# Performance work log

Measured on AMD Instinct MI355X. Metric: run time of the kernel, lower is better.

Reference implementation:

```python
import jax, jax.numpy as jnp
import numpy as np

WIN = 11
SIGMA = 1.5
DATA_RANGE = 2.0
C1 = (0.01 * DATA_RANGE) ** 2
C2 = (0.03 * DATA_RANGE) ** 2


def _gauss_1d():
    x = np.arange(WIN, dtype=np.float32) - WIN // 2
    g = np.exp(-(x ** 2) / (2.0 * SIGMA ** 2))
    return jnp.asarray(g / g.sum(), dtype=jnp.float32)


def _blur(x, g1d):
    c = x.shape[1]
    kh = jnp.broadcast_to(g1d.reshape(1, 1, WIN, 1), (c, 1, WIN, 1))
    kw = jnp.broadcast_to(g1d.reshape(1, 1, 1, WIN), (c, 1, 1, WIN))
    dn = ('NCHW', 'OIHW', 'NCHW')
    p = WIN // 2
    x = jax.lax.conv_general_dilated(x, kh, (1, 1), [(p, p), (0, 0)],
                                     dimension_numbers=dn, feature_group_count=c)
    x = jax.lax.conv_general_dilated(x, kw, (1, 1), [(0, 0), (p, p)],
                                     dimension_numbers=dn, feature_group_count=c)
    return x


def setup_inputs() -> dict:
    key = jax.random.key(0)
    k1, k2 = jax.random.split(key)
    shape = (32, 1, 1024, 1024)
    img1 = jax.random.normal(k1, shape, dtype=jnp.float32)
    img2 = jax.random.normal(k2, shape, dtype=jnp.float32)
    return {"img1": img1, "img2": img2}


def reference(img1, img2):
    g1d = _gauss_1d()
    mu1 = _blur(img1, g1d)
    mu2 = _blur(img2, g1d)
    mu1_sq = mu1 * mu1
    mu2_sq = mu2 * mu2
    mu1_mu2 = mu1 * mu2
    sigma1_sq = _blur(img1 * img1, g1d) - mu1_sq
    sigma2_sq = _blur(img2 * img2, g1d) - mu2_sq
    sigma12 = _blur(img1 * img2, g1d) - mu1_mu2
    ssim_map = ((2.0 * mu1_mu2 + C1) * (2.0 * sigma12 + C2)) / (
        (mu1_sq + mu2_sq + C1) * (sigma1_sq + sigma2_sq + C2))
    return 1.0 - jnp.mean(ssim_map)
```

## Files before the change

### kernel.cpp

```cpp
#include <hip/hip_runtime.h>

typedef float v2f __attribute__((ext_vector_type(2)));

namespace {
constexpr int W = 1024;
constexpr int H = 1024;
constexpr int NIMG = 32;
constexpr int SROWS = 16;
constexpr int NSTRIP = H / SROWS;
constexpr int BLOCK = 256;
constexpr int PLANE4 = 260;

constexpr float C1 = 0.0004f;
constexpr float C2 = 0.0036f;

constexpr float GW[11] = {
    0.00102838f, 0.00759876f, 0.03600077f, 0.10936070f, 0.21300554f,
    0.26601172f,
    0.21300554f, 0.10936070f, 0.03600077f, 0.00759876f, 0.00102838f};
}

__device__ __forceinline__ void lds_barrier() {
  asm volatile("s_waitcnt lgkmcnt(0)" ::: "memory");
  __builtin_amdgcn_s_barrier();
  asm volatile("" ::: "memory");
}

__device__ __forceinline__ void load_uv(const float4* __restrict__ p1,
                                        const float4* __restrict__ p2, int y,
                                        int tid, v2f uv[4]) {
  if ((unsigned)y < (unsigned)H) {
    const float4 a = p1[y * (W / 4) + tid];
    const float4 b = p2[y * (W / 4) + tid];
    uv[0] = (v2f){a.x + b.x, a.x - b.x};
    uv[1] = (v2f){a.y + b.y, a.y - b.y};
    uv[2] = (v2f){a.z + b.z, a.z - b.z};
    uv[3] = (v2f){a.w + b.w, a.w - b.w};
  } else {
#pragma unroll
    for (int c = 0; c < 4; ++c) uv[c] = (v2f){0.f, 0.f};
  }
}

__device__ __forceinline__ void hblur(const float4* __restrict__ P0,
                                      const float4* __restrict__ P1, int tid,
                                      v2f h[4]) {
  v2f t[16];
#pragma unroll
  for (int e = 0; e < 8; ++e) {
    const float4 r = (e & 1) ? P0[tid + (e + 1) / 2] : P1[tid + e / 2];
    t[2 * e + 0] = (v2f){r.x, r.y};
    t[2 * e + 1] = (v2f){r.z, r.w};
  }
#pragma unroll
  for (int m = 0; m < 4; ++m) {
    v2f s = (v2f){GW[0], GW[0]} * t[m + 1];
#pragma unroll
    for (int k = 1; k < 11; ++k)
      s = __builtin_elementwise_fma((v2f){GW[k], GW[k]}, t[m + 1 + k], s);
    h[m] = s;
  }
}

__global__ __launch_bounds__(BLOCK, 4) void ssim_main(
    const float* __restrict__ img1, const float* __restrict__ img2,
    double* __restrict__ ws) {
  __shared__ __align__(16) v2f bufUV[2][2 * PLANE4];
  __shared__ __align__(16) v2f bufSQ[2][2 * PLANE4];
  __shared__ float red[BLOCK / 64];

  const int tid = threadIdx.x;
  const int bid = blockIdx.x;
  const int img = bid / NSTRIP;
  const int strip = bid % NSTRIP;
  const int ys = strip * SROWS;

  const float4* p1 =
      reinterpret_cast<const float4*>(img1) + (size_t)img * (W / 4) * H;
  const float4* p2 =
      reinterpret_cast<const float4*>(img2) + (size_t)img * (W / 4) * H;

  if (tid < 16) {
    const int b = tid & 1, pl = (tid >> 1) & 1, si = tid >> 2;
    const int slot = (si & 1) + ((si >> 1) ? 258 : 0);
    float4* p = reinterpret_cast<float4*>(b ? bufSQ[pl] : bufUV[pl]);
    p[slot] = make_float4(0.f, 0.f, 0.f, 0.f);
  }

  v2f ruv[11][4];
#pragma unroll
  for (int s = 0; s < 10; ++s) load_uv(p1, p2, ys - 5 + s, tid, ruv[s]);
  v2f pf[4];
  load_uv(p1, p2, ys + 5, tid, pf);

  float acc = 0.f;

  for (int ii = 0; ii < SROWS; ++ii) {
#pragma unroll
    for (int c = 0; c < 4; ++c) ruv[10][c] = pf[c];
    load_uv(p1, p2, ys + ii + 6, tid, pf);

    v2f buv[4], bsq[4];
    const v2f g5 = (v2f){GW[5], GW[5]};
#pragma unroll
    for (int c = 0; c < 4; ++c) {
      const v2f x5 = ruv[5][c];
      v2f b = g5 * x5;
      v2f s = g5 * (x5 * x5);
#pragma unroll
      for (int k = 0; k < 5; ++k) {
        const v2f gk = (v2f){GW[k], GW[k]};
        const v2f xa = ruv[k][c];
        const v2f xb = ruv[10 - k][c];
        const v2f p = xa + xb;
        b = __builtin_elementwise_fma(gk, p, b);
        const v2f q = __builtin_elementwise_fma(xb, xb, xa * xa);
        s = __builtin_elementwise_fma(gk, q, s);
      }
      buv[c] = b;
      bsq[c] = s;
    }

    lds_barrier();

    {
      float4* P0 = reinterpret_cast<float4*>(bufUV[0]);
      float4* P1 = reinterpret_cast<float4*>(bufUV[1]);
      P0[tid + 2] = make_float4(buv[0].x, buv[0].y, buv[1].x, buv[1].y);
      P1[tid + 2] = make_float4(buv[2].x, buv[2].y, buv[3].x, buv[3].y);
      float4* Q0 = reinterpret_cast<float4*>(bufSQ[0]);
      float4* Q1 = reinterpret_cast<float4*>(bufSQ[1]);
      Q0[tid + 2] = make_float4(bsq[0].x, bsq[0].y, bsq[1].x, bsq[1].y);
      Q1[tid + 2] = make_float4(bsq[2].x, bsq[2].y, bsq[3].x, bsq[3].y);
    }
    lds_barrier();

    v2f huv[4], hsq[4];
    hblur(reinterpret_cast<const float4*>(bufUV[0]),
          reinterpret_cast<const float4*>(bufUV[1]), tid, huv);
    hblur(reinterpret_cast<const float4*>(bufSQ[0]),
          reinterpret_cast<const float4*>(bufSQ[1]), tid, hsq);

#pragma unroll
    for (int m = 0; m < 4; ++m) {
      const float BU = huv[m].x, BV = huv[m].y;
      const float BU2 = hsq[m].x, BV2 = hsq[m].y;
      const float P = BU * BU, Q = BV * BV;
      const float PmQ = P - Q, PpQ = P + Q;
      const float An = fmaf(0.5f, PmQ, C1);
      const float Bn = fmaf(0.5f, (BU2 - BV2) - PmQ, C2);
      const float Cd = fmaf(0.5f, PpQ, C1);
      const float Dd = fmaf(0.5f, (BU2 + BV2) - PpQ, C2);
      const float num = An * Bn;
      const float den = Cd * Dd;
      float r = __builtin_amdgcn_rcpf(den);
      r = r * fmaf(-den, r, 2.f);
      acc = fmaf(num, r, acc);
    }

#pragma unroll
    for (int k = 0; k < 10; ++k)
#pragma unroll
      for (int c = 0; c < 4; ++c) ruv[k][c] = ruv[k + 1][c];
  }

#pragma unroll
  for (int off = 32; off > 0; off >>= 1) acc += __shfl_down(acc, off, 64);
  if ((tid & 63) == 0) red[tid >> 6] = acc;
  __syncthreads();
  if (tid == 0) {
    float t = 0.f;
#pragma unroll
    for (int wv = 0; wv < BLOCK / 64; ++wv) t += red[wv];
    atomicAdd(ws, (double)t);
  }
}

__global__ void ssim_fin(const double* __restrict__ ws,
                         float* __restrict__ out) {
  out[0] =
      1.0f - (float)(ws[0] * (1.0 / ((double)NIMG * (double)W * (double)H)));
}

extern "C" void kernel_launch(void* const* d_in, const int* in_sizes, int n_in,
                              void* d_out, int out_size, void* d_ws,
                              size_t ws_size, hipStream_t stream) {
  const float* img1 = (const float*)d_in[0];
  const float* img2 = (const float*)d_in[1];
  float* out = (float*)d_out;
  double* ws = (double*)d_ws;

  hipMemsetAsync(d_ws, 0, sizeof(double), stream);
  ssim_main<<<NIMG * NSTRIP, BLOCK, 0, stream>>>(img1, img2, ws);
  ssim_fin<<<1, 1, 0, stream>>>(ws, out);
}
```

Before: 330.7 us.

## Use 512-thread blocks with 2 pixels per thread and taller strips

Each thread now handles 2 columns instead of 4 and loads float2 instead of float4, so a block has 512 threads, and each block covers 32 rows instead of 16. The LDS layout changes to one interleaved float4 plane per quantity, so the horizontal blur reads 7 float4 per thread rather than 8. Taller strips lower the vertical halo reload overhead (10 extra rows per 32 rather than per 16), and fewer registers per thread allow more waves in flight. In exchange the grid has half as many blocks, each thread does less work per row, and the horizontal pass re-reads more overlapping LDS data relative to the output it produces.

New measurement: 352.5 us. +6.6%, slower.

```diff
diff --git a/kernel.cpp b/kernel.cpp
--- a/kernel.cpp
+++ b/kernel.cpp
@@ -6,10 +6,10 @@
 constexpr int W = 1024;
 constexpr int H = 1024;
 constexpr int NIMG = 32;
-constexpr int SROWS = 16;
+constexpr int SROWS = 32;
 constexpr int NSTRIP = H / SROWS;
-constexpr int BLOCK = 256;
-constexpr int PLANE4 = 260;
+constexpr int BLOCK = 512;
+constexpr int NF4 = 520;
 
 constexpr float C1 = 0.0004f;
 constexpr float C2 = 0.0036f;
@@ -26,34 +26,31 @@
   asm volatile("" ::: "memory");
 }
 
-__device__ __forceinline__ void load_uv(const float4* __restrict__ p1,
-                                        const float4* __restrict__ p2, int y,
-                                        int tid, v2f uv[4]) {
+__device__ __forceinline__ void load_uv(const float2* __restrict__ p1,
+                                        const float2* __restrict__ p2, int y,
+                                        int tid, v2f uv[2]) {
   if ((unsigned)y < (unsigned)H) {
-    const float4 a = p1[y * (W / 4) + tid];
-    const float4 b = p2[y * (W / 4) + tid];
+    const float2 a = p1[y * (W / 2) + tid];
+    const float2 b = p2[y * (W / 2) + tid];
     uv[0] = (v2f){a.x + b.x, a.x - b.x};
     uv[1] = (v2f){a.y + b.y, a.y - b.y};
-    uv[2] = (v2f){a.z + b.z, a.z - b.z};
-    uv[3] = (v2f){a.w + b.w, a.w - b.w};
   } else {
-#pragma unroll
-    for (int c = 0; c < 4; ++c) uv[c] = (v2f){0.f, 0.f};
+    uv[0] = (v2f){0.f, 0.f};
+    uv[1] = (v2f){0.f, 0.f};
   }
 }
 
-__device__ __forceinline__ void hblur(const float4* __restrict__ P0,
-                                      const float4* __restrict__ P1, int tid,
-                                      v2f h[4]) {
-  v2f t[16];
+__device__ __forceinline__ void hblur(const float4* __restrict__ B, int tid,
+                                      v2f h[2]) {
+  v2f t[14];
 #pragma unroll
-  for (int e = 0; e < 8; ++e) {
-    const float4 r = (e & 1) ? P0[tid + (e + 1) / 2] : P1[tid + e / 2];
+  for (int e = 0; e < 7; ++e) {
+    const float4 r = B[tid + 1 + e];
     t[2 * e + 0] = (v2f){r.x, r.y};
     t[2 * e + 1] = (v2f){r.z, r.w};
   }
 #pragma unroll
-  for (int m = 0; m < 4; ++m) {
+  for (int m = 0; m < 2; ++m) {
     v2f s = (v2f){GW[0], GW[0]} * t[m + 1];
 #pragma unroll
     for (int k = 1; k < 11; ++k)
@@ -62,11 +59,11 @@
   }
 }
 
-__global__ __launch_bounds__(BLOCK, 4) void ssim_main(
+__global__ __launch_bounds__(BLOCK, 5) void ssim_main(
     const float* __restrict__ img1, const float* __restrict__ img2,
     double* __restrict__ ws) {
-  __shared__ __align__(16) v2f bufUV[2][2 * PLANE4];
-  __shared__ __align__(16) v2f bufSQ[2][2 * PLANE4];
+  __shared__ __align__(16) float4 bufUV[NF4];
+  __shared__ __align__(16) float4 bufSQ[NF4];
   __shared__ float red[BLOCK / 64];
 
   const int tid = threadIdx.x;
@@ -75,35 +72,36 @@
   const int strip = bid % NSTRIP;
   const int ys = strip * SROWS;
 
-  const float4* p1 =
-      reinterpret_cast<const float4*>(img1) + (size_t)img * (W / 4) * H;
-  const float4* p2 =
-      reinterpret_cast<const float4*>(img2) + (size_t)img * (W / 4) * H;
+  const float2* p1 =
+      reinterpret_cast<const float2*>(img1) + (size_t)img * (W / 2) * H;
+  const float2* p2 =
+      reinterpret_cast<const float2*>(img2) + (size_t)img * (W / 2) * H;
 
-  if (tid < 16) {
-    const int b = tid & 1, pl = (tid >> 1) & 1, si = tid >> 2;
-    const int slot = (si & 1) + ((si >> 1) ? 258 : 0);
-    float4* p = reinterpret_cast<float4*>(b ? bufSQ[pl] : bufUV[pl]);
-    p[slot] = make_float4(0.f, 0.f, 0.f, 0.f);
+  if (tid < 4) {
+    const float4 z = make_float4(0.f, 0.f, 0.f, 0.f);
+    bufUV[tid] = z;
+    bufUV[516 + tid] = z;
+    bufSQ[tid] = z;
+    bufSQ[516 + tid] = z;
   }
 
-  v2f ruv[11][4];
+  v2f ruv[11][2];
 #pragma unroll
   for (int s = 0; s < 10; ++s) load_uv(p1, p2, ys - 5 + s, tid, ruv[s]);
-  v2f pf[4];
+  v2f pf[2];
   load_uv(p1, p2, ys + 5, tid, pf);
 
   float acc = 0.f;
 
   for (int ii = 0; ii < SROWS; ++ii) {
-#pragma unroll
-    for (int c = 0; c < 4; ++c) ruv[10][c] = pf[c];
+    ruv[10][0] = pf[0];
+    ruv[10][1] = pf[1];
     load_uv(p1, p2, ys + ii + 6, tid, pf);
 
-    v2f buv[4], bsq[4];
+    v2f buv[2], bsq[2];
     const v2f g5 = (v2f){GW[5], GW[5]};
 #pragma unroll
-    for (int c = 0; c < 4; ++c) {
+    for (int c = 0; c < 2; ++c) {
       const v2f x5 = ruv[5][c];
       v2f b = g5 * x5;
       v2f s = g5 * (x5 * x5);
@@ -123,26 +121,17 @@
 
     lds_barrier();
 
-    {
-      float4* P0 = reinterpret_cast<float4*>(bufUV[0]);
-      float4* P1 = reinterpret_cast<float4*>(bufUV[1]);
-      P0[tid + 2] = make_float4(buv[0].x, buv[0].y, buv[1].x, buv[1].y);
-      P1[tid + 2] = make_float4(buv[2].x, buv[2].y, buv[3].x, buv[3].y);
-      float4* Q0 = reinterpret_cast<float4*>(bufSQ[0]);
-      float4* Q1 = reinterpret_cast<float4*>(bufSQ[1]);
-      Q0[tid + 2] = make_float4(bsq[0].x, bsq[0].y, bsq[1].x, bsq[1].y);
-      Q1[tid + 2] = make_float4(bsq[2].x, bsq[2].y, bsq[3].x, bsq[3].y);
-    }
+    bufUV[tid + 4] = make_float4(buv[0].x, buv[0].y, buv[1].x, buv[1].y);
+    bufSQ[tid + 4] = make_float4(bsq[0].x, bsq[0].y, bsq[1].x, bsq[1].y);
+
     lds_barrier();
 
-    v2f huv[4], hsq[4];
-    hblur(reinterpret_cast<const float4*>(bufUV[0]),
-          reinterpret_cast<const float4*>(bufUV[1]), tid, huv);
-    hblur(reinterpret_cast<const float4*>(bufSQ[0]),
-          reinterpret_cast<const float4*>(bufSQ[1]), tid, hsq);
+    v2f huv[2], hsq[2];
+    hblur(bufUV, tid, huv);
+    hblur(bufSQ, tid, hsq);
 
 #pragma unroll
-    for (int m = 0; m < 4; ++m) {
+    for (int m = 0; m < 2; ++m) {
       const float BU = huv[m].x, BV = huv[m].y;
       const float BU2 = hsq[m].x, BV2 = hsq[m].y;
       const float P = BU * BU, Q = BV * BV;
@@ -159,9 +148,10 @@
     }
 
 #pragma unroll
-    for (int k = 0; k < 10; ++k)
-#pragma unroll
-      for (int c = 0; c < 4; ++c) ruv[k][c] = ruv[k + 1][c];
+    for (int k = 0; k < 10; ++k) {
+      ruv[k][0] = ruv[k + 1][0];
+      ruv[k][1] = ruv[k + 1][1];
+    }
   }
 
 #pragma unroll
```

## Store vertical-blur window in packed bf16 registers and raise occupancy

Applied to the files above, without the earlier changes.

The 11-row sliding window of sum/difference values is converted to bf16 and packed two per 32-bit register, halving its register footprint. Values are unpacked to fp32 by shift/mask before the vertical blur FMAs, and the LDS write ordering is adjusted to match the new packing. Launch bounds go from 4 to 5 blocks per CU to use the freed registers. This trades extra unpack ALU work and reduced input precision for higher occupancy.

Result: slower. 343.9 us (+4.0%).

```diff
diff --git a/kernel.cpp b/kernel.cpp
--- a/kernel.cpp
+++ b/kernel.cpp
@@ -26,19 +26,32 @@
   asm volatile("" ::: "memory");
 }
 
-__device__ __forceinline__ void load_uv(const float4* __restrict__ p1,
-                                        const float4* __restrict__ p2, int y,
-                                        int tid, v2f uv[4]) {
+__device__ __forceinline__ unsigned pk_bf16(float lo, float hi) {
+  unsigned r;
+  asm("v_cvt_pk_bf16_f32 %0, %1, %2" : "=v"(r) : "v"(lo), "v"(hi));
+  return r;
+}
+
+__device__ __forceinline__ v2f unpk(unsigned x) {
+  v2f r;
+  r.x = __uint_as_float(x << 16);
+  r.y = __uint_as_float(x & 0xffff0000u);
+  return r;
+}
+
+__device__ __forceinline__ void load_uv_pk(const float4* __restrict__ p1,
+                                           const float4* __restrict__ p2,
+                                           int y, int tid, unsigned o[4]) {
   if ((unsigned)y < (unsigned)H) {
     const float4 a = p1[y * (W / 4) + tid];
     const float4 b = p2[y * (W / 4) + tid];
-    uv[0] = (v2f){a.x + b.x, a.x - b.x};
-    uv[1] = (v2f){a.y + b.y, a.y - b.y};
-    uv[2] = (v2f){a.z + b.z, a.z - b.z};
-    uv[3] = (v2f){a.w + b.w, a.w - b.w};
+    o[0] = pk_bf16(a.x + b.x, a.y + b.y);
+    o[1] = pk_bf16(a.z + b.z, a.w + b.w);
+    o[2] = pk_bf16(a.x - b.x, a.y - b.y);
+    o[3] = pk_bf16(a.z - b.z, a.w - b.w);
   } else {
 #pragma unroll
-    for (int c = 0; c < 4; ++c) uv[c] = (v2f){0.f, 0.f};
+    for (int c = 0; c < 4; ++c) o[c] = 0u;
   }
 }
 
@@ -62,7 +75,7 @@
   }
 }
 
-__global__ __launch_bounds__(BLOCK, 4) void ssim_main(
+__global__ __launch_bounds__(BLOCK, 5) void ssim_main(
     const float* __restrict__ img1, const float* __restrict__ img2,
     double* __restrict__ ws) {
   __shared__ __align__(16) v2f bufUV[2][2 * PLANE4];
@@ -87,38 +100,38 @@
     p[slot] = make_float4(0.f, 0.f, 0.f, 0.f);
   }
 
-  v2f ruv[11][4];
-#pragma unroll
-  for (int s = 0; s < 10; ++s) load_uv(p1, p2, ys - 5 + s, tid, ruv[s]);
-  v2f pf[4];
-  load_uv(p1, p2, ys + 5, tid, pf);
+  unsigned ruv[11][4];
+#pragma unroll
+  for (int s = 0; s < 10; ++s) load_uv_pk(p1, p2, ys - 5 + s, tid, ruv[s]);
+  unsigned pf[4];
+  load_uv_pk(p1, p2, ys + 5, tid, pf);
 
   float acc = 0.f;
 
   for (int ii = 0; ii < SROWS; ++ii) {
 #pragma unroll
     for (int c = 0; c < 4; ++c) ruv[10][c] = pf[c];
-    load_uv(p1, p2, ys + ii + 6, tid, pf);
-
-    v2f buv[4], bsq[4];
+    load_uv_pk(p1, p2, ys + ii + 6, tid, pf);
+
+    v2f bb[4], ss[4];
     const v2f g5 = (v2f){GW[5], GW[5]};
 #pragma unroll
-    for (int c = 0; c < 4; ++c) {
-      const v2f x5 = ruv[5][c];
+    for (int ch = 0; ch < 4; ++ch) {
+      const v2f x5 = unpk(ruv[5][ch]);
       v2f b = g5 * x5;
       v2f s = g5 * (x5 * x5);
 #pragma unroll
       for (int k = 0; k < 5; ++k) {
         const v2f gk = (v2f){GW[k], GW[k]};
-        const v2f xa = ruv[k][c];
-        const v2f xb = ruv[10 - k][c];
+        const v2f xa = unpk(ruv[k][ch]);
+        const v2f xb = unpk(ruv[10 - k][ch]);
         const v2f p = xa + xb;
         b = __builtin_elementwise_fma(gk, p, b);
         const v2f q = __builtin_elementwise_fma(xb, xb, xa * xa);
         s = __builtin_elementwise_fma(gk, q, s);
       }
-      buv[c] = b;
-      bsq[c] = s;
+      bb[ch] = b;
+      ss[ch] = s;
     }
 
     lds_barrier();
@@ -126,12 +139,12 @@
     {
       float4* P0 = reinterpret_cast<float4*>(bufUV[0]);
       float4* P1 = reinterpret_cast<float4*>(bufUV[1]);
-      P0[tid + 2] = make_float4(buv[0].x, buv[0].y, buv[1].x, buv[1].y);
-      P1[tid + 2] = make_float4(buv[2].x, buv[2].y, buv[3].x, buv[3].y);
+      P0[tid + 2] = make_float4(bb[0].x, bb[2].x, bb[0].y, bb[2].y);
+      P1[tid + 2] = make_float4(bb[1].x, bb[3].x, bb[1].y, bb[3].y);
       float4* Q0 = reinterpret_cast<float4*>(bufSQ[0]);
       float4* Q1 = reinterpret_cast<float4*>(bufSQ[1]);
-      Q0[tid + 2] = make_float4(bsq[0].x, bsq[0].y, bsq[1].x, bsq[1].y);
-      Q1[tid + 2] = make_float4(bsq[2].x, bsq[2].y, bsq[3].x, bsq[3].y);
+      Q0[tid + 2] = make_float4(ss[0].x, ss[2].x, ss[0].y, ss[2].y);
+      Q1[tid + 2] = make_float4(ss[1].x, ss[3].x, ss[1].y, ss[3].y);
     }
     lds_barrier();
 
```
